# Optimization experiments

Hardware: AMD Instinct MI355X
Metric: run time of the kernel (lower is better)

Reference implementation:

```python
import jax, jax.numpy as jnp
import numpy as np

N, E, G = 50000, 800000, 1000
F_IN, H, C = 128, 4, 64  # in-features, heads, per-head channels
NEG_SLOPE = 0.2


def _leaky_relu(v):
    return jnp.where(v > 0, v, NEG_SLOPE * v)


def _gat_conv(x, edge_index, W, a_src, a_dst, bias, heads, out_ch, concat):
    """PyG-style GATConv with add_self_loops=True (eval mode, no dropout)."""
    n = x.shape[0]
    loop = jnp.arange(n, dtype=edge_index.dtype)
    src = jnp.concatenate([edge_index[0], loop])  # [E+N]
    dst = jnp.concatenate([edge_index[1], loop])  # [E+N]
    h = (x @ W).reshape(n, heads, out_ch)          # [N, H, C]
    al_src = jnp.sum(h * a_src, axis=-1)           # [N, H]
    al_dst = jnp.sum(h * a_dst, axis=-1)           # [N, H]
    e = _leaky_relu(al_src[src] + al_dst[dst])     # [E+N, H]
    # segment softmax over incoming edges of each destination node
    m = jax.ops.segment_max(e, dst, num_segments=n)
    ex = jnp.exp(e - jax.lax.stop_gradient(m)[dst])
    denom = jax.ops.segment_sum(ex, dst, num_segments=n)
    alpha = ex / denom[dst]                        # [E+N, H]
    out = jax.ops.segment_sum(h[src] * alpha[..., None], dst, num_segments=n)
    out = out.reshape(n, heads * out_ch) if concat else out.mean(axis=1)
    return out + bias


def _global_mean_pool(x, batch, num_graphs):
    s = jax.ops.segment_sum(x, batch, num_segments=num_graphs)
    cnt = jax.ops.segment_sum(jnp.ones((x.shape[0],), x.dtype), batch, num_segments=num_graphs)
    return s / jnp.maximum(cnt, 1.0)[:, None]


def setup_inputs() -> dict:
    key = jax.random.key(0)
    ks = jax.random.split(key, 20)
    glorot = lambda k, shp: jax.random.normal(k, shp, jnp.float32) * np.sqrt(2.0 / (shp[0] + shp[-1]))
    inp = {
        "x": jax.random.normal(ks[0], (N, F_IN), jnp.float32),
        "edge_index": jax.random.randint(ks[1], (2, E), 0, N, jnp.int32),
        "batch": jnp.sort(jax.random.randint(ks[2], (N,), 0, G, jnp.int32)),
        # conv1: F_IN -> H*C (concat)
        "W1": glorot(ks[3], (F_IN, H * C)),
        "a1_src": glorot(ks[4], (H, C)),
        "a1_dst": glorot(ks[5], (H, C)),
        "b1": jnp.zeros((H * C,), jnp.float32),
        # conv2: H*C -> H*C (concat)
        "W2": glorot(ks[6], (H * C, H * C)),
        "a2_src": glorot(ks[7], (H, C)),
        "a2_dst": glorot(ks[8], (H, C)),
        "b2": jnp.zeros((H * C,), jnp.float32),
        # conv3: H*C -> C (1 head, concat=False)
        "W3": glorot(ks[9], (H * C, C)),
        "a3_src": glorot(ks[10], (1, C)),
        "a3_dst": glorot(ks[11], (1, C)),
        "b3": jnp.zeros((C,), jnp.float32),
        # final linear C -> 1
        "lin_w": glorot(ks[12], (C, 1)),
        "lin_b": jnp.zeros((1,), jnp.float32),
    }
    return inp


def reference(x, edge_index, batch, W1, a1_src, a1_dst, b1, W2, a2_src, a2_dst, b2,
              W3, a3_src, a3_dst, b3, lin_w, lin_b):
    h = jax.nn.elu(_gat_conv(x, edge_index, W1, a1_src, a1_dst, b1, H, C, True))
    h = jax.nn.elu(_gat_conv(h, edge_index, W2, a2_src, a2_dst, b2, H, C, True))
    h = _gat_conv(h, edge_index, W3, a3_src, a3_dst, b3, 1, C, False)
    g = _global_mean_pool(h, batch, G)  # [G, C]
    return g @ lin_w + lin_b            # [G, 1]
```

## Files before the change

### kernel.cpp

```cpp
#include <hip/hip_runtime.h>
#include <cstdint>
#include <cstddef>

#define NEG_SLOPE 0.2f

typedef __attribute__((ext_vector_type(8))) short short8;
typedef __attribute__((ext_vector_type(4))) float f32x4;

__device__ __forceinline__ float lrelu(float v) { return v > 0.f ? v : NEG_SLOPE * v; }

__device__ __forceinline__ unsigned short f2bf(float x) {
    unsigned u = __float_as_uint(x);
    u = (u + 0x7FFFu + ((u >> 16) & 1u)) >> 16;
    return (unsigned short)u;
}
__device__ __forceinline__ float bf2f(unsigned short h) {
    return __uint_as_float(((unsigned)h) << 16);
}

__device__ __forceinline__ void splitbf(float v, unsigned short& hb, unsigned short& lb) {
    unsigned u = __float_as_uint(v);
    hb = (unsigned short)(u >> 16);
    float hf = __uint_as_float(u & 0xFFFF0000u);
    float lf = v - hf;
    lb = (unsigned short)(__float_as_uint(lf) >> 16);
}

__global__ void k_count(const int* __restrict__ ei, int E, int* __restrict__ counts) {
    int i = blockIdx.x * blockDim.x + threadIdx.x;
    if (i < E) atomicAdd(&counts[ei[E + i]], 1);
}

__global__ __launch_bounds__(256) void k_scan_local(const int* __restrict__ counts,
        int* __restrict__ local_ex, int* __restrict__ bsums, int Nn) {
    int base = blockIdx.x * 1024;
    int tid = threadIdx.x;
    int idx = base + tid * 4;
    int4 v = make_int4(0, 0, 0, 0);
    if (idx + 3 < Nn) {
        v = *reinterpret_cast<const int4*>(&counts[idx]);
    } else {
        if (idx + 0 < Nn) v.x = counts[idx + 0];
        if (idx + 1 < Nn) v.y = counts[idx + 1];
        if (idx + 2 < Nn) v.z = counts[idx + 2];
        if (idx + 3 < Nn) v.w = counts[idx + 3];
    }
    int t = v.x + v.y + v.z + v.w;
    int lane = tid & 63, wave = tid >> 6;
    int s = t;
    #pragma unroll
    for (int off = 1; off < 64; off <<= 1) {
        int u = __shfl_up(s, off);
        if (lane >= off) s += u;
    }
    __shared__ int wsum[4];
    if (lane == 63) wsum[wave] = s;
    __syncthreads();
    int wo = 0;
    #pragma unroll
    for (int wv = 0; wv < 4; ++wv) wo += (wv < wave) ? wsum[wv] : 0;
    int ex = wo + s - t;
    int4 o;
    o.x = ex; o.y = ex + v.x; o.z = ex + v.x + v.y; o.w = ex + v.x + v.y + v.z;
    if (idx + 3 < Nn) {
        *reinterpret_cast<int4*>(&local_ex[idx]) = o;
    } else {
        if (idx + 0 < Nn) local_ex[idx + 0] = o.x;
        if (idx + 1 < Nn) local_ex[idx + 1] = o.y;
        if (idx + 2 < Nn) local_ex[idx + 2] = o.z;
        if (idx + 3 < Nn) local_ex[idx + 3] = o.w;
    }
    if (tid == 255) bsums[blockIdx.x] = wo + s;
}

__global__ __launch_bounds__(256) void k_scan_bsums(int* __restrict__ bsums, int nb) {
    int tid = threadIdx.x;
    int v = (tid < nb) ? bsums[tid] : 0;
    int lane = tid & 63, wave = tid >> 6;
    int s = v;
    #pragma unroll
    for (int off = 1; off < 64; off <<= 1) {
        int u = __shfl_up(s, off);
        if (lane >= off) s += u;
    }
    __shared__ int wsum[4];
    if (lane == 63) wsum[wave] = s;
    __syncthreads();
    int wo = 0;
    #pragma unroll
    for (int wv = 0; wv < 4; ++wv) wo += (wv < wave) ? wsum[wv] : 0;
    if (tid < nb) bsums[tid] = wo + s - v;
}

__global__ __launch_bounds__(256) void k_scan_add(const int* __restrict__ local_ex,
        const int* __restrict__ bsums, int* __restrict__ indptr, int* __restrict__ cursor,
        int Nn, int Etot) {
    int i = blockIdx.x * 256 + threadIdx.x;
    if (i < Nn) {
        int val = local_ex[i] + bsums[i >> 10];
        indptr[i] = val;
        cursor[i] = val;
    } else if (i == Nn) {
        indptr[Nn] = Etot;
    }
}

__global__ void k_scatter(const int* __restrict__ ei, int E, int* __restrict__ cursor,
                          int* __restrict__ csr_src) {
    int i = blockIdx.x * blockDim.x + threadIdx.x;
    if (i < E) {
        int s = ei[i], d = ei[E + i];
        int pos = atomicAdd(&cursor[d], 1);
        csr_src[pos] = s;
    }
}

__global__ __launch_bounds__(256) void k_packB(const float* __restrict__ W,
        unsigned short* __restrict__ Ph, unsigned short* __restrict__ Pl, int K, int M) {
    int tid = blockIdx.x * 256 + threadIdx.x;
    int KS8 = K >> 3;
    int total = M * KS8;
    if (tid >= total) return;
    int col = tid / KS8;
    int k = (tid - col * KS8) << 3;
    short8 hv, lv;
    #pragma unroll
    for (int j = 0; j < 8; ++j) {
        float x = W[(size_t)(k + j) * M + col];
        unsigned short hb = f2bf(x);
        hv[j] = (short)hb;
        lv[j] = (short)f2bf(x - bf2f(hb));
    }
    int ct64 = col >> 6, c = col & 63;
    int fb = c >> 4, cl = c & 15;
    int ks = k >> 5, kg = (k >> 3) & 3;
    int lane = cl | (kg << 4);
    size_t off = (((size_t)ct64 * (K >> 5) + ks) * 4 + fb) * 64 + lane;
    *reinterpret_cast<short8*>(Ph + off * 8) = hv;
    *reinterpret_cast<short8*>(Pl + off * 8) = lv;
}

template<int AF, int WR, int WC, bool CONV, int K>
__global__ __launch_bounds__(256) void k_mm(const float* __restrict__ A,
        const unsigned short* __restrict__ Aph, const unsigned short* __restrict__ Apl,
        const unsigned short* __restrict__ Bh, const unsigned short* __restrict__ Bl,
        unsigned short* __restrict__ C, const float* __restrict__ a_src, const float* __restrict__ a_dst,
        float* __restrict__ al_s, float* __restrict__ al_d, int Nrows, int M) {
    constexpr int BF = 4;
    constexpr int BR = WR * AF * 16;
    constexpr int KS = K >> 5;
    int wave = threadIdx.x >> 6, lane = threadIdx.x & 63;
    int wr = wave / WC, wc = wave % WC;
    int rt = blockIdx.x;
    int ct64 = blockIdx.y * WC + wc;
    int rl = lane & 15, kg = lane >> 4;
    const short8* B8h = reinterpret_cast<const short8*>(Bh);
    const short8* B8l = reinterpret_cast<const short8*>(Bl);

    const float* aptr[AF];
    const unsigned short *ahp[AF], *alp[AF];
    #pragma unroll
    for (int f = 0; f < AF; ++f) {
        int row = rt * BR + wr * (AF * 16) + f * 16 + rl;
        if (row > Nrows - 1) row = Nrows - 1;
        if constexpr (CONV) {
            aptr[f] = A + (size_t)row * K + kg * 8;
        } else {
            ahp[f] = Aph + (size_t)row * K + kg * 8;
            alp[f] = Apl + (size_t)row * K + kg * 8;
        }
    }

    f32x4 acc[AF][BF];
    #pragma unroll
    for (int i = 0; i < AF; ++i)
        #pragma unroll
        for (int j = 0; j < BF; ++j)
            acc[i][j] = (f32x4){0.f, 0.f, 0.f, 0.f};

    #pragma unroll
    for (int ks = 0; ks < KS; ++ks) {
        short8 a_h[AF], a_l[AF], b_h[BF], b_l[BF];
        #pragma unroll
        for (int f = 0; f < AF; ++f) {
            if constexpr (CONV) {
                const float* ap = aptr[f] + ks * 32;
                float4 v0 = *reinterpret_cast<const float4*>(ap);
                float4 v1 = *reinterpret_cast<const float4*>(ap + 4);
                float vv[8] = {v0.x, v0.y, v0.z, v0.w, v1.x, v1.y, v1.z, v1.w};
                #pragma unroll
                for (int j = 0; j < 8; ++j) {
                    unsigned short hb, lb;
                    splitbf(vv[j], hb, lb);
                    a_h[f][j] = (short)hb;
                    a_l[f][j] = (short)lb;
                }
            } else {
                a_h[f] = *reinterpret_cast<const short8*>(ahp[f] + ks * 32);
                a_l[f] = *reinterpret_cast<const short8*>(alp[f] + ks * 32);
            }
        }
        #pragma unroll
        for (int f = 0; f < BF; ++f) {
            size_t off = (((size_t)ct64 * KS + ks) * 4 + f) * 64 + lane;
            b_h[f] = B8h[off]; b_l[f] = B8l[off];
        }
        #pragma unroll
        for (int i = 0; i < AF; ++i)
            #pragma unroll
            for (int j = 0; j < BF; ++j) {
                acc[i][j] = __builtin_amdgcn_mfma_f32_16x16x32_bf16(a_l[i], b_h[j], acc[i][j], 0, 0, 0);
                acc[i][j] = __builtin_amdgcn_mfma_f32_16x16x32_bf16(a_h[i], b_l[j], acc[i][j], 0, 0, 0);
                acc[i][j] = __builtin_amdgcn_mfma_f32_16x16x32_bf16(a_h[i], b_h[j], acc[i][j], 0, 0, 0);
            }
    }

    int H = M >> 6;
    int head = ct64;
    int col0 = ct64 * 64;
    int cl = lane & 15, rgrp = lane >> 4;

    float as_[BF], ad_[BF];
    #pragma unroll
    for (int j = 0; j < BF; ++j) {
        as_[j] = a_src[col0 + j * 16 + cl];
        ad_[j] = a_dst[col0 + j * 16 + cl];
    }

    #pragma unroll
    for (int i = 0; i < AF; ++i) {
        int rowb = rt * BR + wr * (AF * 16) + i * 16 + rgrp * 4;
        #pragma unroll
        for (int r = 0; r < 4; ++r) {
            float sv = acc[i][0][r] * as_[0] + acc[i][1][r] * as_[1]
                     + acc[i][2][r] * as_[2] + acc[i][3][r] * as_[3];
            float dv = acc[i][0][r] * ad_[0] + acc[i][1][r] * ad_[1]
                     + acc[i][2][r] * ad_[2] + acc[i][3][r] * ad_[3];
            #pragma unroll
            for (int o = 1; o < 16; o <<= 1) {
                sv += __shfl_xor(sv, o);
                dv += __shfl_xor(dv, o);
            }
            int row = rowb + r;
            if (row < Nrows) {
                unsigned short* cp = &C[(size_t)row * M + col0 + cl];
                cp[0]  = f2bf(acc[i][0][r]);
                cp[16] = f2bf(acc[i][1][r]);
                cp[32] = f2bf(acc[i][2][r]);
                cp[48] = f2bf(acc[i][3][r]);
                if (cl == 0) {
                    al_s[(size_t)row * H + head] = sv;
                    al_d[(size_t)row * H + head] = dv;
                }
            }
        }
    }
}

template <int H, bool ACT, bool POOL>
__global__ __launch_bounds__(256) void k_agg(const unsigned short* __restrict__ hlin,
                      const float* __restrict__ al_s,
                      const float* __restrict__ al_d, const int* __restrict__ indptr,
                      const int* __restrict__ csr_src, const float* __restrict__ bias,
                      unsigned short* __restrict__ out_hi, unsigned short* __restrict__ out_lo,
                      float* __restrict__ outf, const int* __restrict__ batch,
                      int* __restrict__ gcnt, int Nn) {
    constexpr int TOT = H * 64;
    constexpr int VEC = TOT / 64;
    constexpr int CAP = 128;
    __shared__ float sp[4][CAP * H];
    __shared__ int   si[4][CAP];
    int w = threadIdx.x >> 6;
    int lane = threadIdx.x & 63;
    int node = (blockIdx.x * blockDim.x + threadIdx.x) >> 6;
    if (node >= Nn) return;
    int d = node;
    int p0 = indptr[d], p1 = indptr[d + 1];
    int deg = p1 - p0;
    int head = (lane * VEC) >> 6;

    float ad[H], e_self[H];
    if constexpr (H == 4) {
        float4 adv = *reinterpret_cast<const float4*>(&al_d[(size_t)d * 4]);
        float4 asv = *reinterpret_cast<const float4*>(&al_s[(size_t)d * 4]);
        ad[0] = adv.x; ad[1] = adv.y; ad[2] = adv.z; ad[3] = adv.w;
        e_self[0] = lrelu(asv.x + ad[0]); e_self[1] = lrelu(asv.y + ad[1]);
        e_self[2] = lrelu(asv.z + ad[2]); e_self[3] = lrelu(asv.w + ad[3]);
    } else {
        ad[0] = al_d[d];
        e_self[0] = lrelu(al_s[d] + ad[0]);
    }

    float mh, invden, alpha_self;

    if (deg <= CAP) {
        int nb = (deg + 63) >> 6;
        float m[H];
        #pragma unroll
        for (int h = 0; h < H; ++h) m[h] = e_self[h];
        for (int b = 0; b < nb; ++b) {
            int l = b * 64 + lane;
            float e_h[H];
            if (l < deg) {
                int s = csr_src[p0 + l];
                si[w][l] = s;
                if constexpr (H == 4) {
                    float4 sv = *reinterpret_cast<const float4*>(&al_s[(size_t)s * 4]);
                    e_h[0] = lrelu(sv.x + ad[0]); e_h[1] = lrelu(sv.y + ad[1]);
                    e_h[2] = lrelu(sv.z + ad[2]); e_h[3] = lrelu(sv.w + ad[3]);
                } else {
                    e_h[0] = lrelu(al_s[s] + ad[0]);
                }
            } else {
                #pragma unroll
                for (int h = 0; h < H; ++h) e_h[h] = -1e30f;
            }
            #pragma unroll
            for (int h = 0; h < H; ++h) {
                sp[w][l * H + h] = e_h[h];
                m[h] = fmaxf(m[h], e_h[h]);
            }
        }
        #pragma unroll
        for (int h = 0; h < H; ++h)
            #pragma unroll
            for (int off = 1; off < 64; off <<= 1)
                m[h] = fmaxf(m[h], __shfl_xor(m[h], off));
        float den[H];
        #pragma unroll
        for (int h = 0; h < H; ++h) den[h] = 0.f;
        for (int b = 0; b < nb; ++b) {
            int l = b * 64 + lane;
            #pragma unroll
            for (int h = 0; h < H; ++h) {
                float pv = __expf(sp[w][l * H + h] - m[h]);
                sp[w][l * H + h] = pv;
                den[h] += pv;
            }
        }
        #pragma unroll
        for (int h = 0; h < H; ++h) {
            #pragma unroll
            for (int off = 1; off < 64; off <<= 1)
                den[h] += __shfl_xor(den[h], off);
            den[h] += __expf(e_self[h] - m[h]);
        }
        mh = m[head];
        invden = 1.f / den[head];
        alpha_self = __expf(e_self[head] - mh) * invden;

        float4 accv = make_float4(0.f, 0.f, 0.f, 0.f);
        {
            const unsigned short* hp = hlin + (size_t)d * TOT + lane * VEC;
            if constexpr (VEC == 4) {
                ushort4 hv = *reinterpret_cast<const ushort4*>(hp);
                accv.x = alpha_self * bf2f(hv.x); accv.y = alpha_self * bf2f(hv.y);
                accv.z = alpha_self * bf2f(hv.z); accv.w = alpha_self * bf2f(hv.w);
            } else {
                accv.x = alpha_self * bf2f(hp[0]);
            }
        }
        int e = 0;
        for (; e + 8 <= deg; e += 8) {
            int s0 = si[w][e + 0], s1 = si[w][e + 1], s2 = si[w][e + 2], s3 = si[w][e + 3];
            int s4 = si[w][e + 4], s5 = si[w][e + 5], s6 = si[w][e + 6], s7 = si[w][e + 7];
            float a0 = sp[w][(e + 0) * H + head] * invden;
            float a1 = sp[w][(e + 1) * H + head] * invden;
            float a2 = sp[w][(e + 2) * H + head] * invden;
            float a3 = sp[w][(e + 3) * H + head] * invden;
            float a4 = sp[w][(e + 4) * H + head] * invden;
            float a5 = sp[w][(e + 5) * H + head] * invden;
            float a6 = sp[w][(e + 6) * H + head] * invden;
            float a7 = sp[w][(e + 7) * H + head] * invden;
            if constexpr (VEC == 4) {
                ushort4 r0 = *reinterpret_cast<const ushort4*>(hlin + (size_t)s0 * TOT + lane * 4);
                ushort4 r1 = *reinterpret_cast<const ushort4*>(hlin + (size_t)s1 * TOT + lane * 4);
                ushort4 r2 = *reinterpret_cast<const ushort4*>(hlin + (size_t)s2 * TOT + lane * 4);
                ushort4 r3 = *reinterpret_cast<const ushort4*>(hlin + (size_t)s3 * TOT + lane * 4);
                ushort4 r4 = *reinterpret_cast<const ushort4*>(hlin + (size_t)s4 * TOT + lane * 4);
                ushort4 r5 = *reinterpret_cast<const ushort4*>(hlin + (size_t)s5 * TOT + lane * 4);
                ushort4 r6 = *reinterpret_cast<const ushort4*>(hlin + (size_t)s6 * TOT + lane * 4);
                ushort4 r7 = *reinterpret_cast<const ushort4*>(hlin + (size_t)s7 * TOT + lane * 4);
                accv.x += a0*bf2f(r0.x) + a1*bf2f(r1.x) + a2*bf2f(r2.x) + a3*bf2f(r3.x)
                        + a4*bf2f(r4.x) + a5*bf2f(r5.x) + a6*bf2f(r6.x) + a7*bf2f(r7.x);
                accv.y += a0*bf2f(r0.y) + a1*bf2f(r1.y) + a2*bf2f(r2.y) + a3*bf2f(r3.y)
                        + a4*bf2f(r4.y) + a5*bf2f(r5.y) + a6*bf2f(r6.y) + a7*bf2f(r7.y);
                accv.z += a0*bf2f(r0.z) + a1*bf2f(r1.z) + a2*bf2f(r2.z) + a3*bf2f(r3.z)
                        + a4*bf2f(r4.z) + a5*bf2f(r5.z) + a6*bf2f(r6.z) + a7*bf2f(r7.z);
                accv.w += a0*bf2f(r0.w) + a1*bf2f(r1.w) + a2*bf2f(r2.w) + a3*bf2f(r3.w)
                        + a4*bf2f(r4.w) + a5*bf2f(r5.w) + a6*bf2f(r6.w) + a7*bf2f(r7.w);
            } else {
                float r0 = bf2f(hlin[(size_t)s0 * TOT + lane]);
                float r1 = bf2f(hlin[(size_t)s1 * TOT + lane]);
                float r2 = bf2f(hlin[(size_t)s2 * TOT + lane]);
                float r3 = bf2f(hlin[(size_t)s3 * TOT + lane]);
                float r4 = bf2f(hlin[(size_t)s4 * TOT + lane]);
                float r5 = bf2f(hlin[(size_t)s5 * TOT + lane]);
                float r6 = bf2f(hlin[(size_t)s6 * TOT + lane]);
                float r7 = bf2f(hlin[(size_t)s7 * TOT + lane]);
                accv.x += a0*r0 + a1*r1 + a2*r2 + a3*r3 + a4*r4 + a5*r5 + a6*r6 + a7*r7;
            }
        }
        for (; e + 4 <= deg; e += 4) {
            int s0 = si[w][e + 0], s1 = si[w][e + 1];
            int s2 = si[w][e + 2], s3 = si[w][e + 3];
            float a0 = sp[w][(e + 0) * H + head] * invden;
            float a1 = sp[w][(e + 1) * H + head] * invden;
            float a2 = sp[w][(e + 2) * H + head] * invden;
            float a3 = sp[w][(e + 3) * H + head] * invden;
            if constexpr (VEC == 4) {
                ushort4 r0 = *reinterpret_cast<const ushort4*>(hlin + (size_t)s0 * TOT + lane * 4);
                ushort4 r1 = *reinterpret_cast<const ushort4*>(hlin + (size_t)s1 * TOT + lane * 4);
                ushort4 r2 = *reinterpret_cast<const ushort4*>(hlin + (size_t)s2 * TOT + lane * 4);
                ushort4 r3 = *reinterpret_cast<const ushort4*>(hlin + (size_t)s3 * TOT + lane * 4);
                accv.x += a0*bf2f(r0.x) + a1*bf2f(r1.x) + a2*bf2f(r2.x) + a3*bf2f(r3.x);
                accv.y += a0*bf2f(r0.y) + a1*bf2f(r1.y) + a2*bf2f(r2.y) + a3*bf2f(r3.y);
                accv.z += a0*bf2f(r0.z) + a1*bf2f(r1.z) + a2*bf2f(r2.z) + a3*bf2f(r3.z);
                accv.w += a0*bf2f(r0.w) + a1*bf2f(r1.w) + a2*bf2f(r2.w) + a3*bf2f(r3.w);
            } else {
                float r0 = bf2f(hlin[(size_t)s0 * TOT + lane]);
                float r1 = bf2f(hlin[(size_t)s1 * TOT + lane]);
                float r2 = bf2f(hlin[(size_t)s2 * TOT + lane]);
                float r3 = bf2f(hlin[(size_t)s3 * TOT + lane]);
                accv.x += a0 * r0 + a1 * r1 + a2 * r2 + a3 * r3;
            }
        }
        for (; e < deg; ++e) {
            int s = si[w][e];
            float a = sp[w][e * H + head] * invden;
            if constexpr (VEC == 4) {
                ushort4 rv = *reinterpret_cast<const ushort4*>(hlin + (size_t)s * TOT + lane * 4);
                accv.x += a * bf2f(rv.x); accv.y += a * bf2f(rv.y);
                accv.z += a * bf2f(rv.z); accv.w += a * bf2f(rv.w);
            } else {
                accv.x += a * bf2f(hlin[(size_t)s * TOT + lane]);
            }
        }
        if constexpr (VEC == 4) {
            int c0 = lane * 4;
            accv.x += bias[c0 + 0]; accv.y += bias[c0 + 1];
            accv.z += bias[c0 + 2]; accv.w += bias[c0 + 3];
            if (ACT) {
                accv.x = accv.x > 0.f ? accv.x : expm1f(accv.x);
                accv.y = accv.y > 0.f ? accv.y : expm1f(accv.y);
                accv.z = accv.z > 0.f ? accv.z : expm1f(accv.z);
                accv.w = accv.w > 0.f ? accv.w : expm1f(accv.w);
            }
            ushort4 hv, lv;
            splitbf(accv.x, hv.x, lv.x);
            splitbf(accv.y, hv.y, lv.y);
            splitbf(accv.z, hv.z, lv.z);
            splitbf(accv.w, hv.w, lv.w);
            *reinterpret_cast<ushort4*>(&out_hi[(size_t)d * TOT + c0]) = hv;
            *reinterpret_cast<ushort4*>(&out_lo[(size_t)d * TOT + c0]) = lv;
        } else {
            float o = accv.x + bias[lane];
            if (ACT) o = o > 0.f ? o : expm1f(o);
            if constexpr (POOL) {
                int g = batch[d];
                atomicAdd(&outf[(size_t)g * 64 + lane], o);
                if (lane == 0) atomicAdd(&gcnt[g], 1);
            } else {
                unsigned short hb, lb;
                splitbf(o, hb, lb);
                out_hi[(size_t)d * TOT + lane] = hb;
                out_lo[(size_t)d * TOT + lane] = lb;
            }
        }
        return;
    }

    {
        float adh = ad[head];
        float es = e_self[head];
        float m = es;
        for (int e = p0; e < p1; ++e) {
            int s = csr_src[e];
            m = fmaxf(m, lrelu(al_s[(size_t)s * H + head] + adh));
        }
        float den = __expf(es - m);
        for (int e = p0; e < p1; ++e) {
            int s = csr_src[e];
            den += __expf(lrelu(al_s[(size_t)s * H + head] + adh) - m);
        }
        den = 1.f / den;
        float accv[VEC] = {};
        {
            float alpha = __expf(es - m) * den;
            const unsigned short* hp = hlin + (size_t)d * TOT + lane * VEC;
            #pragma unroll
            for (int v = 0; v < VEC; ++v) accv[v] = alpha * bf2f(hp[v]);
        }
        for (int e = p0; e < p1; ++e) {
            int s = csr_src[e];
            float alpha = __expf(lrelu(al_s[(size_t)s * H + head] + adh) - m) * den;
            const unsigned short* hp = hlin + (size_t)s * TOT + lane * VEC;
            #pragma unroll
            for (int v = 0; v < VEC; ++v) accv[v] += alpha * bf2f(hp[v]);
        }
        #pragma unroll
        for (int v = 0; v < VEC; ++v) {
            int c = lane * VEC + v;
            float o = accv[v] + bias[c];
            if (ACT) o = o > 0.f ? o : expm1f(o);
            accv[v] = o;
        }
        if constexpr (POOL) {
            int g = batch[d];
            atomicAdd(&outf[(size_t)g * 64 + lane], accv[0]);
            if (lane == 0) atomicAdd(&gcnt[g], 1);
        } else {
            #pragma unroll
            for (int v = 0; v < VEC; ++v) {
                unsigned short hb, lb;
                splitbf(accv[v], hb, lb);
                out_hi[(size_t)d * TOT + lane * VEC + v] = hb;
                out_lo[(size_t)d * TOT + lane * VEC + v] = lb;
            }
        }
    }
}

__global__ void k_final(const float* __restrict__ gsum, const int* __restrict__ gcnt,
                        const float* __restrict__ lin_w, const float* __restrict__ lin_b,
                        float* __restrict__ out, int Gn) {
    int g = (blockIdx.x * blockDim.x + threadIdx.x) >> 6;
    int lane = threadIdx.x & 63;
    if (g >= Gn) return;
    float cnt = (float)gcnt[g];
    float inv = 1.f / fmaxf(cnt, 1.f);
    float v = gsum[(size_t)g * 64 + lane] * inv * lin_w[lane];
    #pragma unroll
    for (int off = 32; off >= 1; off >>= 1) v += __shfl_xor(v, off);
    if (lane == 0) out[g] = v + lin_b[0];
}

extern "C" void kernel_launch(void* const* d_in, const int* in_sizes, int n_in,
                              void* d_out, int out_size, void* d_ws, size_t ws_size,
                              hipStream_t stream) {
    const float* x    = (const float*)d_in[0];
    const int*   ei   = (const int*)d_in[1];
    const int*   batch= (const int*)d_in[2];
    const float* W1   = (const float*)d_in[3];
    const float* a1s  = (const float*)d_in[4];
    const float* a1d  = (const float*)d_in[5];
    const float* b1   = (const float*)d_in[6];
    const float* W2   = (const float*)d_in[7];
    const float* a2s  = (const float*)d_in[8];
    const float* a2d  = (const float*)d_in[9];
    const float* b2   = (const float*)d_in[10];
    const float* W3   = (const float*)d_in[11];
    const float* a3s  = (const float*)d_in[12];
    const float* a3d  = (const float*)d_in[13];
    const float* b3   = (const float*)d_in[14];
    const float* lw   = (const float*)d_in[15];
    const float* lb   = (const float*)d_in[16];

    int N = in_sizes[0] / 128;
    int E = in_sizes[1] / 2;
    int G = out_size;
    int RT32 = (N + 31) >> 5;
    int RT64 = (N + 63) >> 6;
    int Np = ((N + 127) >> 7) * 128;
    int NB = (N + 1023) >> 10;

    char* p = (char*)d_ws;
    auto alloc = [&](size_t bytes) {
        char* r = p;
        p += (bytes + 255) & ~(size_t)255;
        return r;
    };
    unsigned short* hbuf = (unsigned short*)alloc((size_t)Np * 256 * 2);
    unsigned short* aggh = (unsigned short*)alloc((size_t)Np * 256 * 2);
    unsigned short* aggl = (unsigned short*)alloc((size_t)Np * 256 * 2);
    unsigned short* pB1h = (unsigned short*)alloc((size_t)128 * 256 * 2);
    unsigned short* pB1l = (unsigned short*)alloc((size_t)128 * 256 * 2);
    unsigned short* pB2h = (unsigned short*)alloc((size_t)256 * 256 * 2);
    unsigned short* pB2l = (unsigned short*)alloc((size_t)256 * 256 * 2);
    unsigned short* pB3h = (unsigned short*)alloc((size_t)256 * 64 * 2);
    unsigned short* pB3l = (unsigned short*)alloc((size_t)256 * 64 * 2);
    float* al_s  = (float*)alloc((size_t)N * 4 * 4);
    float* al_d  = (float*)alloc((size_t)N * 4 * 4);
    int* indptr  = (int*)alloc((size_t)(N + 1) * 4);
    int* counts  = (int*)alloc((size_t)N * 4);
    int* cursor  = (int*)alloc((size_t)N * 4);
    int* lex     = (int*)alloc((size_t)N * 4);
    int* bsums   = (int*)alloc((size_t)256 * 4);
    int* csr     = (int*)alloc((size_t)E * 4);
    float* gsum  = (float*)alloc((size_t)G * 64 * 4);
    int* gcnt    = (int*)alloc((size_t)G * 4);
    if ((size_t)(p - (char*)d_ws) > ws_size) return;

    hipMemsetAsync(counts, 0, (size_t)N * 4, stream);
    hipMemsetAsync(gsum, 0, (size_t)G * 64 * 4, stream);
    hipMemsetAsync(gcnt, 0, (size_t)G * 4, stream);

    k_packB<<<(256 * (128 >> 3) + 255) / 256, 256, 0, stream>>>(W1, pB1h, pB1l, 128, 256);
    k_packB<<<(256 * (256 >> 3) + 255) / 256, 256, 0, stream>>>(W2, pB2h, pB2l, 256, 256);
    k_packB<<<(64 * (256 >> 3) + 255) / 256, 256, 0, stream>>>(W3, pB3h, pB3l, 256, 64);

    int eb = (E + 255) / 256;
    k_count<<<eb, 256, 0, stream>>>(ei, E, counts);
    k_scan_local<<<NB, 256, 0, stream>>>(counts, lex, bsums, N);
    k_scan_bsums<<<1, 256, 0, stream>>>(bsums, NB);
    k_scan_add<<<(N + 1 + 255) / 256, 256, 0, stream>>>(lex, bsums, indptr, cursor, N, E);
    k_scatter<<<eb, 256, 0, stream>>>(ei, E, cursor, csr);

    int wb = (N * 64 + 255) / 256;

    k_mm<2, 1, 4, true, 128><<<dim3(RT32, 1), 256, 0, stream>>>(x, nullptr, nullptr,
        pB1h, pB1l, hbuf, a1s, a1d, al_s, al_d, N, 256);
    k_agg<4, true, false><<<wb, 256, 0, stream>>>(hbuf, al_s, al_d, indptr, csr, b1,
        aggh, aggl, nullptr, nullptr, nullptr, N);

    k_mm<2, 1, 4, false, 256><<<dim3(RT32, 1), 256, 0, stream>>>(nullptr, aggh, aggl,
        pB2h, pB2l, hbuf, a2s, a2d, al_s, al_d, N, 256);
    k_agg<4, true, false><<<wb, 256, 0, stream>>>(hbuf, al_s, al_d, indptr, csr, b2,
        aggh, aggl, nullptr, nullptr, nullptr, N);

    k_mm<1, 4, 1, false, 256><<<dim3(RT64, 1), 256, 0, stream>>>(nullptr, aggh, aggl,
        pB3h, pB3l, hbuf, a3s, a3d, al_s, al_d, N, 64);
    k_agg<1, false, true><<<wb, 256, 0, stream>>>(hbuf, al_s, al_d, indptr, csr, b3,
        nullptr, nullptr, gsum, batch, gcnt, N);

    int fb = (G * 64 + 255) / 256;
    k_final<<<fb, 256, 0, stream>>>(gsum, gcnt, lw, lb, (float*)d_out, G);
}
```

Measured before the change: 416.8 us.

## Fuse weight-pack and scan kernels, restructure per-head softmax in aggregation

Merges the three weight-packing launches into one kernel and folds the block-sums scan into the scan-add kernel, cutting kernel launches. In the aggregation kernel, the per-edge softmax max and denominator are now computed per head by lane groups, each handling only its own head, instead of every lane reducing all heads. Normalization by the denominator is deferred to a single multiply at the end rather than applied per edge. Each scan-add block now redundantly rescans the block sums, and that inline scan only covers up to 64 block sums.

```diff
diff --git a/kernel.cpp b/kernel.cpp
--- a/kernel.cpp
+++ b/kernel.cpp
@@ -73,31 +73,25 @@
     if (tid == 255) bsums[blockIdx.x] = wo + s;
 }
 
-__global__ __launch_bounds__(256) void k_scan_bsums(int* __restrict__ bsums, int nb) {
-    int tid = threadIdx.x;
-    int v = (tid < nb) ? bsums[tid] : 0;
-    int lane = tid & 63, wave = tid >> 6;
-    int s = v;
-    #pragma unroll
-    for (int off = 1; off < 64; off <<= 1) {
-        int u = __shfl_up(s, off);
-        if (lane >= off) s += u;
-    }
-    __shared__ int wsum[4];
-    if (lane == 63) wsum[wave] = s;
-    __syncthreads();
-    int wo = 0;
-    #pragma unroll
-    for (int wv = 0; wv < 4; ++wv) wo += (wv < wave) ? wsum[wv] : 0;
-    if (tid < nb) bsums[tid] = wo + s - v;
-}
-
 __global__ __launch_bounds__(256) void k_scan_add(const int* __restrict__ local_ex,
         const int* __restrict__ bsums, int* __restrict__ indptr, int* __restrict__ cursor,
-        int Nn, int Etot) {
-    int i = blockIdx.x * 256 + threadIdx.x;
+        int Nn, int Etot, int NB) {
+    __shared__ int pref[64];
+    int tid = threadIdx.x;
+    if (tid < 64) {
+        int v = (tid < NB) ? bsums[tid] : 0;
+        int s = v;
+        #pragma unroll
+        for (int off = 1; off < 64; off <<= 1) {
+            int u = __shfl_up(s, off);
+            if ((tid & 63) >= off) s += u;
+        }
+        pref[tid] = s - v;
+    }
+    __syncthreads();
+    int i = blockIdx.x * 256 + tid;
     if (i < Nn) {
-        int val = local_ex[i] + bsums[i >> 10];
+        int val = local_ex[i] + pref[i >> 10];
         indptr[i] = val;
         cursor[i] = val;
     } else if (i == Nn) {
@@ -115,12 +109,10 @@
     }
 }
 
-__global__ __launch_bounds__(256) void k_packB(const float* __restrict__ W,
-        unsigned short* __restrict__ Ph, unsigned short* __restrict__ Pl, int K, int M) {
-    int tid = blockIdx.x * 256 + threadIdx.x;
+__device__ __forceinline__ void packB_one(const float* __restrict__ W,
+        unsigned short* __restrict__ Ph, unsigned short* __restrict__ Pl,
+        int K, int M, int tid) {
     int KS8 = K >> 3;
-    int total = M * KS8;
-    if (tid >= total) return;
     int col = tid / KS8;
     int k = (tid - col * KS8) << 3;
     short8 hv, lv;
@@ -138,6 +130,17 @@
     size_t off = (((size_t)ct64 * (K >> 5) + ks) * 4 + fb) * 64 + lane;
     *reinterpret_cast<short8*>(Ph + off * 8) = hv;
     *reinterpret_cast<short8*>(Pl + off * 8) = lv;
+}
+
+__global__ __launch_bounds__(256) void k_packB3(const float* __restrict__ W1,
+        const float* __restrict__ W2, const float* __restrict__ W3,
+        unsigned short* p1h, unsigned short* p1l,
+        unsigned short* p2h, unsigned short* p2l,
+        unsigned short* p3h, unsigned short* p3l) {
+    int tid = blockIdx.x * 256 + threadIdx.x;
+    if (tid < 4096)        packB_one(W1, p1h, p1l, 128, 256, tid);
+    else if (tid < 12288)  packB_one(W2, p2h, p2l, 256, 256, tid - 4096);
+    else if (tid < 14336)  packB_one(W3, p3h, p3l, 256, 64, tid - 12288);
 }
 
 template<int AF, int WR, int WC, bool CONV, int K>
@@ -268,6 +271,7 @@
     constexpr int TOT = H * 64;
     constexpr int VEC = TOT / 64;
     constexpr int CAP = 128;
+    constexpr int GRPW = 64 / H;
     __shared__ float sp[4][CAP * H];
     __shared__ int   si[4][CAP];
     int w = threadIdx.x >> 6;
@@ -291,13 +295,8 @@
         e_self[0] = lrelu(al_s[d] + ad[0]);
     }
 
-    float mh, invden, alpha_self;
-
     if (deg <= CAP) {
         int nb = (deg + 63) >> 6;
-        float m[H];
-        #pragma unroll
-        for (int h = 0; h < H; ++h) m[h] = e_self[h];
         for (int b = 0; b < nb; ++b) {
             int l = b * 64 + lane;
             float e_h[H];
@@ -316,62 +315,52 @@
                 for (int h = 0; h < H; ++h) e_h[h] = -1e30f;
             }
             #pragma unroll
-            for (int h = 0; h < H; ++h) {
-                sp[w][l * H + h] = e_h[h];
-                m[h] = fmaxf(m[h], e_h[h]);
-            }
-        }
-        #pragma unroll
-        for (int h = 0; h < H; ++h)
-            #pragma unroll
-            for (int off = 1; off < 64; off <<= 1)
-                m[h] = fmaxf(m[h], __shfl_xor(m[h], off));
-        float den[H];
-        #pragma unroll
-        for (int h = 0; h < H; ++h) den[h] = 0.f;
-        for (int b = 0; b < nb; ++b) {
-            int l = b * 64 + lane;
-            #pragma unroll
-            for (int h = 0; h < H; ++h) {
-                float pv = __expf(sp[w][l * H + h] - m[h]);
-                sp[w][l * H + h] = pv;
-                den[h] += pv;
-            }
-        }
-        #pragma unroll
-        for (int h = 0; h < H; ++h) {
-            #pragma unroll
-            for (int off = 1; off < 64; off <<= 1)
-                den[h] += __shfl_xor(den[h], off);
-            den[h] += __expf(e_self[h] - m[h]);
-        }
-        mh = m[head];
-        invden = 1.f / den[head];
-        alpha_self = __expf(e_self[head] - mh) * invden;
+            for (int h = 0; h < H; ++h) sp[w][l * H + h] = e_h[h];
+        }
+        int li = lane & (GRPW - 1);
+        int tot = nb * 64;
+        float mg = e_self[head];
+        for (int l = li; l < tot; l += GRPW)
+            mg = fmaxf(mg, sp[w][l * H + head]);
+        #pragma unroll
+        for (int o = 1; o < GRPW; o <<= 1)
+            mg = fmaxf(mg, __shfl_xor(mg, o));
+        float deng = 0.f;
+        for (int l = li; l < tot; l += GRPW) {
+            float pv = __expf(sp[w][l * H + head] - mg);
+            sp[w][l * H + head] = pv;
+            deng += pv;
+        }
+        #pragma unroll
+        for (int o = 1; o < GRPW; o <<= 1)
+            deng += __shfl_xor(deng, o);
+        float esx = __expf(e_self[head] - mg);
+        deng += esx;
+        float invden = 1.f / deng;
 
         float4 accv = make_float4(0.f, 0.f, 0.f, 0.f);
         {
             const unsigned short* hp = hlin + (size_t)d * TOT + lane * VEC;
             if constexpr (VEC == 4) {
                 ushort4 hv = *reinterpret_cast<const ushort4*>(hp);
-                accv.x = alpha_self * bf2f(hv.x); accv.y = alpha_self * bf2f(hv.y);
-                accv.z = alpha_self * bf2f(hv.z); accv.w = alpha_self * bf2f(hv.w);
+                accv.x = esx * bf2f(hv.x); accv.y = esx * bf2f(hv.y);
+                accv.z = esx * bf2f(hv.z); accv.w = esx * bf2f(hv.w);
             } else {
-                accv.x = alpha_self * bf2f(hp[0]);
+                accv.x = esx * bf2f(hp[0]);
             }
         }
         int e = 0;
         for (; e + 8 <= deg; e += 8) {
             int s0 = si[w][e + 0], s1 = si[w][e + 1], s2 = si[w][e + 2], s3 = si[w][e + 3];
             int s4 = si[w][e + 4], s5 = si[w][e + 5], s6 = si[w][e + 6], s7 = si[w][e + 7];
-            float a0 = sp[w][(e + 0) * H + head] * invden;
-            float a1 = sp[w][(e + 1) * H + head] * invden;
-            float a2 = sp[w][(e + 2) * H + head] * invden;
-            float a3 = sp[w][(e + 3) * H + head] * invden;
-            float a4 = sp[w][(e + 4) * H + head] * invden;
-            float a5 = sp[w][(e + 5) * H + head] * invden;
-            float a6 = sp[w][(e + 6) * H + head] * invden;
-            float a7 = sp[w][(e + 7) * H + head] * invden;
+            float a0 = sp[w][(e + 0) * H + head];
+            float a1 = sp[w][(e + 1) * H + head];
+            float a2 = sp[w][(e + 2) * H + head];
+            float a3 = sp[w][(e + 3) * H + head];
+            float a4 = sp[w][(e + 4) * H + head];
+            float a5 = sp[w][(e + 5) * H + head];
+            float a6 = sp[w][(e + 6) * H + head];
+            float a7 = sp[w][(e + 7) * H + head];
             if constexpr (VEC == 4) {
                 ushort4 r0 = *reinterpret_cast<const ushort4*>(hlin + (size_t)s0 * TOT + lane * 4);
                 ushort4 r1 = *reinterpret_cast<const ushort4*>(hlin + (size_t)s1 * TOT + lane * 4);
@@ -404,10 +393,10 @@
         for (; e + 4 <= deg; e += 4) {
             int s0 = si[w][e + 0], s1 = si[w][e + 1];
             int s2 = si[w][e + 2], s3 = si[w][e + 3];
-            float a0 = sp[w][(e + 0) * H + head] * invden;
-            float a1 = sp[w][(e + 1) * H + head] * invden;
-            float a2 = sp[w][(e + 2) * H + head] * invden;
-            float a3 = sp[w][(e + 3) * H + head] * invden;
+            float a0 = sp[w][(e + 0) * H + head];
+            float a1 = sp[w][(e + 1) * H + head];
+            float a2 = sp[w][(e + 2) * H + head];
+            float a3 = sp[w][(e + 3) * H + head];
             if constexpr (VEC == 4) {
                 ushort4 r0 = *reinterpret_cast<const ushort4*>(hlin + (size_t)s0 * TOT + lane * 4);
                 ushort4 r1 = *reinterpret_cast<const ushort4*>(hlin + (size_t)s1 * TOT + lane * 4);
@@ -427,7 +416,7 @@
         }
         for (; e < deg; ++e) {
             int s = si[w][e];
-            float a = sp[w][e * H + head] * invden;
+            float a = sp[w][e * H + head];
             if constexpr (VEC == 4) {
                 ushort4 rv = *reinterpret_cast<const ushort4*>(hlin + (size_t)s * TOT + lane * 4);
                 accv.x += a * bf2f(rv.x); accv.y += a * bf2f(rv.y);
@@ -438,8 +427,10 @@
         }
         if constexpr (VEC == 4) {
             int c0 = lane * 4;
-            accv.x += bias[c0 + 0]; accv.y += bias[c0 + 1];
-            accv.z += bias[c0 + 2]; accv.w += bias[c0 + 3];
+            accv.x = accv.x * invden + bias[c0 + 0];
+            accv.y = accv.y * invden + bias[c0 + 1];
+            accv.z = accv.z * invden + bias[c0 + 2];
+            accv.w = accv.w * invden + bias[c0 + 3];
             if (ACT) {
                 accv.x = accv.x > 0.f ? accv.x : expm1f(accv.x);
                 accv.y = accv.y > 0.f ? accv.y : expm1f(accv.y);
@@ -454,7 +445,7 @@
             *reinterpret_cast<ushort4*>(&out_hi[(size_t)d * TOT + c0]) = hv;
             *reinterpret_cast<ushort4*>(&out_lo[(size_t)d * TOT + c0]) = lv;
         } else {
-            float o = accv.x + bias[lane];
+            float o = accv.x * invden + bias[lane];
             if (ACT) o = o > 0.f ? o : expm1f(o);
             if constexpr (POOL) {
                 int g = batch[d];
@@ -595,15 +586,13 @@
     hipMemsetAsync(gsum, 0, (size_t)G * 64 * 4, stream);
     hipMemsetAsync(gcnt, 0, (size_t)G * 4, stream);
 
-    k_packB<<<(256 * (128 >> 3) + 255) / 256, 256, 0, stream>>>(W1, pB1h, pB1l, 128, 256);
-    k_packB<<<(256 * (256 >> 3) + 255) / 256, 256, 0, stream>>>(W2, pB2h, pB2l, 256, 256);
-    k_packB<<<(64 * (256 >> 3) + 255) / 256, 256, 0, stream>>>(W3, pB3h, pB3l, 256, 64);
+    k_packB3<<<(14336 + 255) / 256, 256, 0, stream>>>(W1, W2, W3,
+        pB1h, pB1l, pB2h, pB2l, pB3h, pB3l);
 
     int eb = (E + 255) / 256;
     k_count<<<eb, 256, 0, stream>>>(ei, E, counts);
     k_scan_local<<<NB, 256, 0, stream>>>(counts, lex, bsums, N);
-    k_scan_bsums<<<1, 256, 0, stream>>>(bsums, NB);
-    k_scan_add<<<(N + 1 + 255) / 256, 256, 0, stream>>>(lex, bsums, indptr, cursor, N, E);
+    k_scan_add<<<(N + 1 + 255) / 256, 256, 0, stream>>>(lex, bsums, indptr, cursor, N, E, NB);
     k_scatter<<<eb, 256, 0, stream>>>(ei, E, cursor, csr);
 
     int wb = (N * 64 + 255) / 256;
```

New measurement: 407.3 us. -2.3%, faster.
